# Performance work log

Measured on AMD Instinct MI355X. Metric: run time of the kernel, lower is better.

Reference implementation:

```python
import jax, jax.numpy as jnp
import numpy as np


def setup_inputs() -> dict:
    key = jax.random.key(0)
    kq, kk, kv = jax.random.split(key, 3)
    B, H, SQ, KV, D = 2, 16, 2048, 4096, 128
    q = jax.random.normal(kq, (B, H, SQ, D), dtype=jnp.float32)
    k = jax.random.normal(kk, (B, H, KV, D), dtype=jnp.float32)
    v = jax.random.normal(kv, (B, H, KV, D), dtype=jnp.float32)
    return {"q": q, "k": k, "v": v}


def reference(q, k, v):
    # Faithful to F.scaled_dot_product_attention with a boolean mask that is
    # True for the first half of KV positions (masked positions -> -inf).
    KV = k.shape[2]
    D = q.shape[-1]
    scale = 1.0 / jnp.sqrt(jnp.asarray(D, dtype=q.dtype))
    # [B, H, Sq, KV] scores
    scores = jnp.einsum("bhqd,bhkd->bhqk", q, k) * scale
    kv_pos = jnp.arange(KV)
    mask = (kv_pos < KV // 2)[None, None, None, :]  # [1,1,1,KV]
    neg_inf = jnp.asarray(jnp.finfo(scores.dtype).min, dtype=scores.dtype)
    scores = jnp.where(mask, scores, neg_inf)
    attn = jax.nn.softmax(scores, axis=-1)
    return jnp.einsum("bhqk,bhkd->bhqd", attn, v)
```

## Files before the change

kernel.cpp:

```cpp
#include <hip/hip_runtime.h>


#define NT 32

typedef _Float16 half8  __attribute__((ext_vector_type(8)));
typedef __fp16   fp16x2 __attribute__((ext_vector_type(2)));
typedef float    floatx4 __attribute__((ext_vector_type(4)));
typedef unsigned int uint;
typedef uint     uintx4 __attribute__((ext_vector_type(4)));

#if __has_builtin(__builtin_amdgcn_exp2f)
#define EXP2(x) __builtin_amdgcn_exp2f(x)
#else
#define EXP2(x) exp2f(x)
#endif

union H2U { fp16x2 h; uint u; };
union H8U { uint u[4]; half8 h; };

static __device__ __forceinline__ uint pk(float a, float b) {
    H2U z; z.h = __builtin_amdgcn_cvt_pkrtz(a, b); return z.u;
}

#define KH_BH 524288u
#define VT_BASE 16777216u
#define VT_BH 524288u

#define GLOAD_LDS16(g, l)                                                     \
    __builtin_amdgcn_global_load_lds(                                         \
        (const __attribute__((address_space(1))) uint*)(const void*)(g),      \
        (__attribute__((address_space(3))) uint*)(void*)(l), 16, 0, 0)

__global__ __launch_bounds__(256)
void cvt_kernel(const float* __restrict__ K, const float* __restrict__ V,
                char* __restrict__ ws) {
    const int bid = blockIdx.x;
    const int bh  = bid >> 5;
    const int kv0 = (bid & 31) * 64;
    const int t   = threadIdx.x;

    const float* Kb = K + (size_t)bh * 4096 * 128 + (size_t)kv0 * 128;
    const float* Vb = V + (size_t)bh * 4096 * 128 + (size_t)kv0 * 128;
    char* Khb = ws + (size_t)bh * KH_BH + (size_t)kv0 * 256;
    char* Vtb = ws + VT_BASE + (size_t)bh * VT_BH;

    {
        const int c16 = t & 15;
        #pragma unroll
        for (int rnd = 0; rnd < 4; ++rnd) {
            const int r = rnd * 16 + (t >> 4);
            const float* src = Kb + (size_t)r * 128 + c16 * 8;
            floatx4 a = *(const floatx4*)src;
            floatx4 b = *(const floatx4*)(src + 4);
            H8U hh;
            hh.u[0] = pk(a[0], a[1]); hh.u[1] = pk(a[2], a[3]);
            hh.u[2] = pk(b[0], b[1]); hh.u[3] = pk(b[2], b[3]);
            const int key = (r & 7) ^ ((r >> 1) & 4);
            *(half8*)(Khb + r * 256 + 16 * (c16 ^ key)) = hh.h;
        }
    }

    __shared__ __align__(16) uint U[128 * 32];
    {
        const int dpos = t & 31;
        const int k3   = t >> 5;
        #pragma unroll
        for (int rnd = 0; rnd < 4; ++rnd) {
            const int kvp = rnd * 8 + k3;
            floatx4 a = *(const floatx4*)(Vb + (size_t)(2 * kvp) * 128 + 4 * dpos);
            floatx4 b = *(const floatx4*)(Vb + (size_t)(2 * kvp + 1) * 128 + 4 * dpos);
            #pragma unroll
            for (int e = 0; e < 4; ++e) {
                const int d   = 4 * dpos + e;
                const int col = (kvp & 3) |
                                ((((kvp >> 2) ^ d ^ (d >> 2)) & 7) << 2);
                U[d * 32 + col] = pk(a[e], b[e]);
            }
        }
    }
    __syncthreads();
    {
        const int s = t & 7;
        #pragma unroll
        for (int rnd = 0; rnd < 4; ++rnd) {
            const int d = rnd * 32 + (t >> 3);
            uintx4 u = *(const uintx4*)&U[d * 32 + 4 * s];
            *(uintx4*)(Vtb + (size_t)d * 4096 + (size_t)kv0 * 2 +
                       16 * ((s ^ (d >> 2)) & 7)) = u;
        }
    }
}

__global__ __launch_bounds__(512, 2)
void fa_kernel(const float* __restrict__ Q, float* __restrict__ O,
               const char* __restrict__ ws) {
    const float SCALE = 0.08838834764831845f * 1.4426950408889634f;

    __shared__ __align__(16) char smem[98304];

    const int t    = threadIdx.x;
    const int lane = t & 63;
    const int w    = t >> 6;
    const int wq   = w & 3;
    const int dh   = w >> 2;
    const int c    = lane & 15;
    const int qd   = lane >> 4;

    const int idx  = blockIdx.x;
    const int xcd  = idx & 7;
    const int slot = idx >> 3;
    const int qt   = slot & 7;
    const int bh   = xcd + 8 * (slot >> 3);
    const int q0   = qt * 256;

    const float* Qb  = Q + (size_t)bh * 2048 * 128;
    float*       Ob  = O + (size_t)bh * 2048 * 128;
    const char*  Khb = ws + (size_t)bh * KH_BH;
    const char*  Vtb = ws + VT_BASE + (size_t)bh * VT_BH;

    char* const kb0 = smem;
    char* const vb0 = smem + 32768;
    char* const pex = smem + 65536;

    #define ISSUE_K(kv0_, dst_)                                                  \
        { _Pragma("unroll")                                                      \
          for (int j = 0; j < 2; ++j) {                                          \
              const int i = 2 * w + j;                                           \
              const char* g = Khb + (size_t)(kv0_) * 256 +                       \
                              (size_t)(4 * i + (lane >> 4)) * 256 + (lane & 15) * 16; \
              GLOAD_LDS16(g, (dst_) + i * 1024); } }
    #define ISSUE_V(kv0_, dst_)                                                  \
        { _Pragma("unroll")                                                      \
          for (int j = 0; j < 2; ++j) {                                          \
              const int i = 2 * w + j;                                           \
              const char* g = Vtb + (size_t)(8 * i + (lane >> 3)) * 4096 +       \
                              (size_t)(kv0_) * 2 + (lane & 7) * 16;              \
              GLOAD_LDS16(g, (dst_) + i * 1024); } }

    ISSUE_K(0, kb0);
    ISSUE_V(0, vb0);

    half8 bq[4][4];
    #pragma unroll
    for (int m = 0; m < 4; ++m) {
        #pragma unroll
        for (int s = 0; s < 4; ++s) {
            const int row = q0 + 64 * wq + 16 * m + c;
            const float* p = Qb + (size_t)row * 128 + 32 * s + 8 * qd;
            floatx4 x = *(const floatx4*)p;
            floatx4 y = *(const floatx4*)(p + 4);
            H8U hh;
            hh.u[0] = pk(x[0] * SCALE, x[1] * SCALE);
            hh.u[1] = pk(x[2] * SCALE, x[3] * SCALE);
            hh.u[2] = pk(y[0] * SCALE, y[1] * SCALE);
            hh.u[3] = pk(y[2] * SCALE, y[3] * SCALE);
            bq[m][s] = hh.h;
        }
    }

    floatx4 o[4][4];
    float lsum[4] = {0.f, 0.f, 0.f, 0.f};
    #pragma unroll
    for (int m = 0; m < 4; ++m)
        #pragma unroll
        for (int dt = 0; dt < 4; ++dt) o[m][dt] = (floatx4){0.f, 0.f, 0.f, 0.f};

    char* const pex_own = pex + (w << 12) + (qd << 8) + (c << 4);
    const char* const pex_sib = pex + ((w ^ 4) << 12) + (qd << 8) + (c << 4);

    __syncthreads();

    for (int kt = 0; kt < NT; ++kt) {
        const int cur = kt & 1;
        char* kcur = kb0 + cur * 16384;
        char* vcur = vb0 + cur * 16384;
        if (kt + 1 < NT) {
            ISSUE_K((kt + 1) * 64, kb0 + (1 - cur) * 16384);
            ISSUE_V((kt + 1) * 64, vb0 + (1 - cur) * 16384);
        }

        floatx4 st[2][4];
        #pragma unroll
        for (int g = 0; g < 2; ++g)
            #pragma unroll
            for (int m = 0; m < 4; ++m) st[g][m] = (floatx4){0.f, 0.f, 0.f, 0.f};

        __builtin_amdgcn_s_setprio(1);
        #pragma unroll
        for (int g = 0; g < 2; ++g) {
            const int row = 32 * dh + 8 * (c >> 2) + 4 * g + (c & 3);
            const int key = (row & 7) ^ ((row >> 1) & 4);
            #pragma unroll
            for (int s = 0; s < 4; ++s) {
                half8 ka = *(const half8*)(kcur + row * 256 + 16 * ((4 * s + qd) ^ key));
                #pragma unroll
                for (int m = 0; m < 4; ++m)
                    st[g][m] = __builtin_amdgcn_mfma_f32_16x16x32_f16(ka, bq[m][s], st[g][m], 0, 0, 0);
            }
        }
        __builtin_amdgcn_s_setprio(0);

        half8 pb[4];
        #pragma unroll
        for (int m = 0; m < 4; ++m) {
            const float p0 = EXP2(st[0][m][0]);
            const float p1 = EXP2(st[0][m][1]);
            const float p2 = EXP2(st[0][m][2]);
            const float p3 = EXP2(st[0][m][3]);
            const float p4 = EXP2(st[1][m][0]);
            const float p5 = EXP2(st[1][m][1]);
            const float p6 = EXP2(st[1][m][2]);
            const float p7 = EXP2(st[1][m][3]);
            lsum[m] += ((p0 + p1) + (p2 + p3)) + ((p4 + p5) + (p6 + p7));
            H8U hh;
            hh.u[0] = pk(p0, p1); hh.u[1] = pk(p2, p3);
            hh.u[2] = pk(p4, p5); hh.u[3] = pk(p6, p7);
            pb[m] = hh.h;
            *(half8*)(pex_own + (m << 10)) = pb[m];
        }

        asm volatile("s_waitcnt lgkmcnt(0)" ::: "memory");
        __builtin_amdgcn_s_barrier();
        asm volatile("" ::: "memory");

        half8 ps[4];
        #pragma unroll
        for (int m = 0; m < 4; ++m)
            ps[m] = *(const half8*)(pex_sib + (m << 10));

        __builtin_amdgcn_s_setprio(1);
        #pragma unroll
        for (int dt = 0; dt < 4; ++dt) {
            const int d = 64 * dh + 16 * dt + c;
            half8 va_own = *(const half8*)(vcur + d * 128 + 16 * ((4 * dh + qd) ^ (d & 7)));
            half8 va_sib = *(const half8*)(vcur + d * 128 + 16 * ((4 * (dh ^ 1) + qd) ^ (d & 7)));
            #pragma unroll
            for (int m = 0; m < 4; ++m) {
                o[m][dt] = __builtin_amdgcn_mfma_f32_16x16x32_f16(va_own, pb[m], o[m][dt], 0, 0, 0);
                o[m][dt] = __builtin_amdgcn_mfma_f32_16x16x32_f16(va_sib, ps[m], o[m][dt], 0, 0, 0);
            }
        }
        __builtin_amdgcn_s_setprio(0);

        __syncthreads();
    }

    #pragma unroll
    for (int m = 0; m < 4; ++m) {
        lsum[m] += __shfl_xor(lsum[m], 16, 64);
        lsum[m] += __shfl_xor(lsum[m], 32, 64);
    }
    float* lbuf = (float*)pex;
    if (qd == 0) {
        #pragma unroll
        for (int m = 0; m < 4; ++m)
            lbuf[dh * 256 + 64 * wq + 16 * m + c] = lsum[m];
    }
    __syncthreads();
    #pragma unroll
    for (int m = 0; m < 4; ++m) {
        const int qrow = 64 * wq + 16 * m + c;
        const float invl = 1.0f / (lbuf[qrow] + lbuf[256 + qrow]);
        #pragma unroll
        for (int dt = 0; dt < 4; ++dt) {
            floatx4 r = o[m][dt];
            r[0] *= invl; r[1] *= invl; r[2] *= invl; r[3] *= invl;
            *(floatx4*)&Ob[(size_t)(q0 + qrow) * 128 + 64 * dh + 16 * dt + 4 * qd] = r;
        }
    }
}

extern "C" void kernel_launch(void* const* d_in, const int* in_sizes, int n_in,
                              void* d_out, int out_size, void* d_ws, size_t ws_size,
                              hipStream_t stream) {
    const float* q = (const float*)d_in[0];
    const float* k = (const float*)d_in[1];
    const float* v = (const float*)d_in[2];
    float* out = (float*)d_out;
    char* ws = (char*)d_ws;
    cvt_kernel<<<dim3(1024), dim3(256), 0, stream>>>(k, v, ws);
    fa_kernel<<<dim3(256), dim3(512), 0, stream>>>(q, out, ws);
}
```

Measured before the change: 228.9 us.

## Split PV by KV half per wave pair and reduce partial outputs at end

Each wave pair previously swapped its P fragments through shared memory every KV tile, which needed an extra barrier per iteration. Now each wave multiplies only its own P slice against all 128 V columns, holding partial accumulators for the full head dimension. The two partial sums are added once at the end through a shared-memory exchange. This removes the per-tile P exchange, its barrier and 32KB of LDS. In exchange it doubles the output accumulator registers per wave, which risks spilling or lower occupancy under the 512x2 launch bound.

```diff
diff --git a/kernel.cpp b/kernel.cpp
--- a/kernel.cpp
+++ b/kernel.cpp
@@ -96,7 +96,7 @@
                const char* __restrict__ ws) {
     const float SCALE = 0.08838834764831845f * 1.4426950408889634f;
 
-    __shared__ __align__(16) char smem[98304];
+    __shared__ __align__(16) char smem[65536];
 
     const int t    = threadIdx.x;
     const int lane = t & 63;
@@ -120,7 +120,6 @@
 
     char* const kb0 = smem;
     char* const vb0 = smem + 32768;
-    char* const pex = smem + 65536;
 
     #define ISSUE_K(kv0_, dst_)                                                  \
         { _Pragma("unroll")                                                      \
@@ -158,15 +157,12 @@
         }
     }
 
-    floatx4 o[4][4];
+    floatx4 o[4][8];
     float lsum[4] = {0.f, 0.f, 0.f, 0.f};
     #pragma unroll
     for (int m = 0; m < 4; ++m)
         #pragma unroll
-        for (int dt = 0; dt < 4; ++dt) o[m][dt] = (floatx4){0.f, 0.f, 0.f, 0.f};
-
-    char* const pex_own = pex + (w << 12) + (qd << 8) + (c << 4);
-    const char* const pex_sib = pex + ((w ^ 4) << 12) + (qd << 8) + (c << 4);
+        for (int dt = 0; dt < 8; ++dt) o[m][dt] = (floatx4){0.f, 0.f, 0.f, 0.f};
 
     __syncthreads();
 
@@ -216,29 +212,16 @@
             hh.u[0] = pk(p0, p1); hh.u[1] = pk(p2, p3);
             hh.u[2] = pk(p4, p5); hh.u[3] = pk(p6, p7);
             pb[m] = hh.h;
-            *(half8*)(pex_own + (m << 10)) = pb[m];
-        }
-
-        asm volatile("s_waitcnt lgkmcnt(0)" ::: "memory");
-        __builtin_amdgcn_s_barrier();
-        asm volatile("" ::: "memory");
-
-        half8 ps[4];
-        #pragma unroll
-        for (int m = 0; m < 4; ++m)
-            ps[m] = *(const half8*)(pex_sib + (m << 10));
+        }
 
         __builtin_amdgcn_s_setprio(1);
         #pragma unroll
-        for (int dt = 0; dt < 4; ++dt) {
-            const int d = 64 * dh + 16 * dt + c;
-            half8 va_own = *(const half8*)(vcur + d * 128 + 16 * ((4 * dh + qd) ^ (d & 7)));
-            half8 va_sib = *(const half8*)(vcur + d * 128 + 16 * ((4 * (dh ^ 1) + qd) ^ (d & 7)));
-            #pragma unroll
-            for (int m = 0; m < 4; ++m) {
-                o[m][dt] = __builtin_amdgcn_mfma_f32_16x16x32_f16(va_own, pb[m], o[m][dt], 0, 0, 0);
-                o[m][dt] = __builtin_amdgcn_mfma_f32_16x16x32_f16(va_sib, ps[m], o[m][dt], 0, 0, 0);
-            }
+        for (int dt = 0; dt < 8; ++dt) {
+            const int d = 16 * dt + c;
+            half8 va = *(const half8*)(vcur + d * 128 + 16 * ((4 * dh + qd) ^ (d & 7)));
+            #pragma unroll
+            for (int m = 0; m < 4; ++m)
+                o[m][dt] = __builtin_amdgcn_mfma_f32_16x16x32_f16(va, pb[m], o[m][dt], 0, 0, 0);
         }
         __builtin_amdgcn_s_setprio(0);
 
@@ -250,23 +233,34 @@
         lsum[m] += __shfl_xor(lsum[m], 16, 64);
         lsum[m] += __shfl_xor(lsum[m], 32, 64);
     }
-    float* lbuf = (float*)pex;
+    float* lbuf = (float*)smem;
+    char* const xch = smem + 32768;
     if (qd == 0) {
         #pragma unroll
         for (int m = 0; m < 4; ++m)
             lbuf[dh * 256 + 64 * wq + 16 * m + c] = lsum[m];
     }
     __syncthreads();
+
     #pragma unroll
     for (int m = 0; m < 4; ++m) {
         const int qrow = 64 * wq + 16 * m + c;
         const float invl = 1.0f / (lbuf[qrow] + lbuf[256 + qrow]);
         #pragma unroll
-        for (int dt = 0; dt < 4; ++dt) {
-            floatx4 r = o[m][dt];
+        for (int dtl = 0; dtl < 4; ++dtl) {
+            const int dt_w = 4 * (1 - dh) + dtl;
+            *(floatx4*)(xch + (w << 12) + (dtl << 10) + (lane << 4)) = o[m][dt_w];
+        }
+        __syncthreads();
+        #pragma unroll
+        for (int dtl = 0; dtl < 4; ++dtl) {
+            const int dt_o = 4 * dh + dtl;
+            floatx4 r = o[m][dt_o] +
+                *(const floatx4*)(xch + ((w ^ 4) << 12) + (dtl << 10) + (lane << 4));
             r[0] *= invl; r[1] *= invl; r[2] *= invl; r[3] *= invl;
-            *(floatx4*)&Ob[(size_t)(q0 + qrow) * 128 + 64 * dh + 16 * dt + 4 * qd] = r;
-        }
+            *(floatx4*)&Ob[(size_t)(q0 + qrow) * 128 + 16 * dt_o + 4 * qd] = r;
+        }
+        __syncthreads();
     }
 }
 
```

After: 525.0 us. 129% more time.

## Triple-buffer K/V tiles in LDS with explicit vmcnt waits

Applied to the files above, without the earlier changes.

Replaces the double-buffered K/V ring with a three-slot ring, prefetching two tiles ahead. Each iteration now waits on the outstanding global-to-LDS loads with an explicit s_waitcnt vmcnt(4) plus a raw barrier, in place of the trailing __syncthreads. The aim is to hide more global-load latency behind the MFMA work and to avoid draining all loads every iteration. In exchange, LDS use grows to 128KB per block, and correctness now depends on the hand-counted vmcnt matching the number of issued loads.

```diff
diff --git a/kernel.cpp b/kernel.cpp
--- a/kernel.cpp
+++ b/kernel.cpp
@@ -96,7 +96,7 @@
                const char* __restrict__ ws) {
     const float SCALE = 0.08838834764831845f * 1.4426950408889634f;
 
-    __shared__ __align__(16) char smem[98304];
+    __shared__ __align__(16) char smem[131072];
 
     const int t    = threadIdx.x;
     const int lane = t & 63;
@@ -118,9 +118,7 @@
     const char*  Khb = ws + (size_t)bh * KH_BH;
     const char*  Vtb = ws + VT_BASE + (size_t)bh * VT_BH;
 
-    char* const kb0 = smem;
-    char* const vb0 = smem + 32768;
-    char* const pex = smem + 65536;
+    char* const pexb = smem + 98304;
 
     #define ISSUE_K(kv0_, dst_)                                                  \
         { _Pragma("unroll")                                                      \
@@ -137,8 +135,10 @@
                               (size_t)(kv0_) * 2 + (lane & 7) * 16;              \
               GLOAD_LDS16(g, (dst_) + i * 1024); } }
 
-    ISSUE_K(0, kb0);
-    ISSUE_V(0, vb0);
+    ISSUE_K(0,  smem);
+    ISSUE_V(0,  smem + 16384);
+    ISSUE_K(64, smem + 32768);
+    ISSUE_V(64, smem + 49152);
 
     half8 bq[4][4];
     #pragma unroll
@@ -165,19 +165,25 @@
         #pragma unroll
         for (int dt = 0; dt < 4; ++dt) o[m][dt] = (floatx4){0.f, 0.f, 0.f, 0.f};
 
-    char* const pex_own = pex + (w << 12) + (qd << 8) + (c << 4);
-    const char* const pex_sib = pex + ((w ^ 4) << 12) + (qd << 8) + (c << 4);
-
-    __syncthreads();
+    char* const pex_own = pexb + (w << 12) + (qd << 8) + (c << 4);
+    const char* const pex_sib = pexb + ((w ^ 4) << 12) + (qd << 8) + (c << 4);
+
+    int slc = 0;
+    int sli = 2;
 
     for (int kt = 0; kt < NT; ++kt) {
-        const int cur = kt & 1;
-        char* kcur = kb0 + cur * 16384;
-        char* vcur = vb0 + cur * 16384;
-        if (kt + 1 < NT) {
-            ISSUE_K((kt + 1) * 64, kb0 + (1 - cur) * 16384);
-            ISSUE_V((kt + 1) * 64, vb0 + (1 - cur) * 16384);
-        }
+        if (kt + 1 < NT) { asm volatile("s_waitcnt vmcnt(4)" ::: "memory"); }
+        else             { asm volatile("s_waitcnt vmcnt(0)" ::: "memory"); }
+        __builtin_amdgcn_s_barrier();
+        asm volatile("" ::: "memory");
+
+        if (kt + 2 < NT) {
+            char* ib = smem + sli * 32768;
+            ISSUE_K((kt + 2) * 64, ib);
+            ISSUE_V((kt + 2) * 64, ib + 16384);
+        }
+        char* kcur = smem + slc * 32768;
+        char* vcur = kcur + 16384;
 
         floatx4 st[2][4];
         #pragma unroll
@@ -242,15 +248,18 @@
         }
         __builtin_amdgcn_s_setprio(0);
 
-        __syncthreads();
-    }
+        slc = (slc == 2) ? 0 : slc + 1;
+        sli = (sli == 2) ? 0 : sli + 1;
+    }
+
+    __syncthreads();
 
     #pragma unroll
     for (int m = 0; m < 4; ++m) {
         lsum[m] += __shfl_xor(lsum[m], 16, 64);
         lsum[m] += __shfl_xor(lsum[m], 32, 64);
     }
-    float* lbuf = (float*)pex;
+    float* lbuf = (float*)pexb;
     if (qd == 0) {
         #pragma unroll
         for (int m = 0; m < 4; ++m)
```

New measurement: 227.9 us. Within noise of the previous version (-0.4%).
